# Kernel optimization log

Measured on AMD Instinct MI355X. Metric: run time of the kernel, lower is better.

The kernel has to match this reference:

```python
import jax, jax.numpy as jnp
import numpy as np

B, I, H = 16384, 512, 512


def setup_inputs() -> dict:
    key = jax.random.key(0)
    ks = jax.random.split(key, 10)
    inputs = jax.random.normal(ks[0], (B, I), dtype=jnp.float32)
    state = jax.random.normal(ks[1], (B, 2 * H), dtype=jnp.float32)
    # xavier_uniform for w_ih: U(-a, a), a = sqrt(6 / (fan_in + fan_out))
    a = float(np.sqrt(6.0 / (2 * H + I)))
    w_ih = jax.random.uniform(ks[2], (2 * H, I), jnp.float32, -a, a)
    b_h = jnp.zeros((H,), jnp.float32)
    pi = float(np.pi)
    d1 = jax.random.uniform(ks[3], (H,), jnp.float32, -pi, pi)
    d2 = jax.random.uniform(ks[4], (H,), jnp.float32, -pi, pi)
    d3 = jax.random.uniform(ks[5], (H,), jnp.float32, -pi, pi)
    re1 = jax.random.uniform(ks[6], (H,), jnp.float32, -1.0, 1.0)
    im1 = jax.random.uniform(ks[7], (H,), jnp.float32, -1.0, 1.0)
    re2 = jax.random.uniform(ks[8], (H,), jnp.float32, -1.0, 1.0)
    im2 = jax.random.uniform(ks[9], (H,), jnp.float32, -1.0, 1.0)
    perm = jnp.asarray(np.random.default_rng(0).permutation(H), dtype=jnp.int32)
    return {"inputs": inputs, "state": state, "w_ih": w_ih, "b_h": b_h,
            "d1": d1, "d2": d2, "d3": d3,
            "re1": re1, "im1": im1, "re2": re2, "im2": im2, "perm": perm}


def _diag_mul(w, z):
    # multiply by exp(i*w) built as complex(cos w, sin w), as in the original
    return jax.lax.complex(jnp.cos(w), jnp.sin(w)) * z


def _reflect(re, im, z):
    # z - (2/||v||^2) * (z @ conj(v)) outer v   (faithful to original matmuls)
    v = jax.lax.complex(re, im)                 # [H]
    vz = z @ jnp.conj(v)                        # [B]
    factor = 2.0 / jnp.sum(re * re + im * im)   # real scalar
    return z - factor * vz[:, None] * v[None, :]


def _modrelu(z, b):
    norm = jnp.abs(z)
    scale = jax.nn.relu(norm + b) / (norm + 1e-6)
    return z * scale


def reference(inputs, state, w_ih, b_h, d1, d2, d3, re1, im1, re2, im2, perm):
    inputs_mul = inputs @ w_ih.T                                  # [B, 2H]
    z_in = jax.lax.complex(inputs_mul[:, :H], inputs_mul[:, H:])  # [B, H] c64
    state_c = jax.lax.complex(state[:, :H], state[:, H:])
    # Unitary chain (computed in original forward, but its result `preact` is
    # never used for the returned state -- faithfully reproduced).
    s = _diag_mul(d1, state_c)
    s = jnp.fft.fft(s, axis=-1)
    s = _reflect(re1, im1, s)
    s = s[:, perm]                 # column permutation (z.T[P].T)
    s = _diag_mul(d2, s)
    s = jnp.fft.ifft(s, axis=-1)
    s = _reflect(re2, im2, s)
    s = _diag_mul(d3, s)
    preact = z_in + s              # dead in original; kept for fidelity
    new_state_c = _modrelu(z_in, b_h)
    return jnp.concatenate([jnp.real(new_state_c), jnp.imag(new_state_c)], axis=1)
```

## Files before the change

### kernel.cpp

```cpp
#include <hip/hip_runtime.h>
#include <hip/hip_bf16.h>


typedef __attribute__((ext_vector_type(8))) short bf16x8;
typedef __attribute__((ext_vector_type(4))) float f32x4;

#define BM 128
#define BK 64
#define KDIM 512
#define NDIM 1024
#define NKT 8

#define VMCNT(n) asm volatile("s_waitcnt vmcnt(" #n ")" ::: "memory")
#define LGKM(n)  asm volatile("s_waitcnt lgkmcnt(" #n ")" ::: "memory")

__device__ __forceinline__ unsigned short f2bf(float f) {
    unsigned u = __builtin_bit_cast(unsigned, f);
    u += 0x7fffu + ((u >> 16) & 1u);
    return (unsigned short)(u >> 16);
}

__global__ __launch_bounds__(256) void cvt_w(const float* __restrict__ W,
                                             unsigned short* __restrict__ Wbf, int n4) {
    int i = blockIdx.x * blockDim.x + threadIdx.x;
    int stride = gridDim.x * blockDim.x;
    for (; i < n4; i += stride) {
        float4 v = reinterpret_cast<const float4*>(W)[i];
        ushort4 o;
        o.x = f2bf(v.x); o.y = f2bf(v.y); o.z = f2bf(v.z); o.w = f2bf(v.w);
        reinterpret_cast<ushort4*>(Wbf)[i] = o;
    }
}

__device__ __forceinline__ void gload_lds16(const void* g, void* l) {
    __builtin_amdgcn_global_load_lds(
        (const __attribute__((address_space(1))) unsigned int*)g,
        (__attribute__((address_space(3))) unsigned int*)l, 16, 0, 0);
}

__device__ __forceinline__ unsigned cvtpk(float lo, float hi) {
    unsigned r;
    asm("v_cvt_pk_bf16_f32 %0, %1, %2" : "=v"(r) : "v"(lo), "v"(hi));
    return r;
}

__global__ __launch_bounds__(256, 2) void gemm_modrelu(
    const float* __restrict__ A,
    const unsigned short* __restrict__ W,
    const float* __restrict__ bh,
    float* __restrict__ out)
{
    __shared__ unsigned short At[2][BM * BK];
    __shared__ unsigned short Bt[2][BM * BK];

    const int tid = threadIdx.x;
    const int w   = tid >> 6;
    const int l   = tid & 63;
    const int l15 = l & 15;
    const int l4  = l >> 4;
    const int wm  = w >> 1;
    const int wn  = w & 1;

    const int bx = blockIdx.x;
    const int lg = (bx & 7) * 128 + (bx >> 3);
    const int mb = lg >> 3;
    const int cb = lg & 7;

    const int arow0 = tid >> 4;
    const int aseg  = tid & 15;
    const int aswz  = (arow0 & 7) << 3;
    const float4* gA = reinterpret_cast<const float4*>(A) + (size_t)(mb * BM) * (KDIM / 4);
    const int abase = arow0 * (KDIM / 4) + aseg;

    const int srow = l >> 3;
    const int sseg = (l & 7) ^ srow;
    const unsigned short* gb[4];
    int ldso[4];
#pragma unroll
    for (int is = 0; is < 4; ++is) {
        int row  = w * 32 + is * 8 + srow;
        int wrow = (row >> 6) * 512 + cb * 64 + (row & 63);
        gb[is]   = W + (size_t)wrow * KDIM + sseg * 8;
        ldso[is] = (w * 32 + is * 8) * BK;
    }

    float4 ra[3][8];
    auto load_a = [&](int kt, int set) {
#pragma unroll
        for (int s = 0; s < 8; ++s)
            ra[set][s] = gA[(size_t)s * 16 * (KDIM / 4) + abase + kt * (BK / 4)];
    };
    auto write_a = [&](int buf, int set) {
#pragma unroll
        for (int s = 0; s < 8; ++s) {
            uint2 o;
            o.x = cvtpk(ra[set][s].x, ra[set][s].y);
            o.y = cvtpk(ra[set][s].z, ra[set][s].w);
            int row = s * 16 + arow0;
            *reinterpret_cast<uint2*>(&At[buf][row * BK + ((aseg * 4) ^ aswz)]) = o;
        }
    };
    auto stage_b = [&](int kt, int buf) {
#pragma unroll
        for (int is = 0; is < 4; ++is)
            gload_lds16(gb[is] + kt * BK, &Bt[buf][ldso[is]]);
    };

    f32x4 acc[4][4];
#pragma unroll
    for (int i = 0; i < 4; ++i)
#pragma unroll
        for (int j = 0; j < 4; ++j) acc[i][j] = f32x4{0.f, 0.f, 0.f, 0.f};

    load_a(0, 0);
    load_a(1, 1);
    stage_b(0, 0);
    load_a(2, 2);
    stage_b(1, 1);
    VMCNT(24);
    write_a(0, 0);
    VMCNT(12);
    LGKM(0);
    __builtin_amdgcn_s_barrier();

#pragma unroll
    for (int kt = 0; kt < NKT; ++kt) {
        const int buf = kt & 1;

        bf16x8 af[4], bf[4];
#pragma unroll
        for (int i = 0; i < 4; ++i) {
            int row = wm * 64 + i * 16 + l15;
            af[i] = *(const bf16x8*)(&At[buf][row * BK + (l4 ^ (row & 7)) * 8]);
        }
#pragma unroll
        for (int j = 0; j < 4; ++j) {
            int row = (j >> 1) * 64 + wn * 32 + (j & 1) * 16 + l15;
            bf[j] = *(const bf16x8*)(&Bt[buf][row * BK + (l4 ^ (row & 7)) * 8]);
        }
        if (kt + 1 < NKT) write_a(buf ^ 1, (kt + 1) % 3);
        if (kt + 3 < NKT) load_a(kt + 3, (kt + 3) % 3);

        if (kt + 1 < NKT) { LGKM(8); } else { LGKM(0); }
        __builtin_amdgcn_sched_barrier(0);
        __builtin_amdgcn_s_setprio(1);
#pragma unroll
        for (int i = 0; i < 4; ++i)
#pragma unroll
            for (int j = 0; j < 4; ++j)
                acc[i][j] = __builtin_amdgcn_mfma_f32_16x16x32_bf16(
                    af[i], bf[j], acc[i][j], 0, 0, 0);
        __builtin_amdgcn_s_setprio(0);

#pragma unroll
        for (int i = 0; i < 4; ++i) {
            int row = wm * 64 + i * 16 + l15;
            af[i] = *(const bf16x8*)(&At[buf][row * BK + ((4 + l4) ^ (row & 7)) * 8]);
        }
#pragma unroll
        for (int j = 0; j < 4; ++j) {
            int row = (j >> 1) * 64 + wn * 32 + (j & 1) * 16 + l15;
            bf[j] = *(const bf16x8*)(&Bt[buf][row * BK + ((4 + l4) ^ (row & 7)) * 8]);
        }
        LGKM(0);
        __builtin_amdgcn_sched_barrier(0);
        __builtin_amdgcn_s_setprio(1);
#pragma unroll
        for (int i = 0; i < 4; ++i)
#pragma unroll
            for (int j = 0; j < 4; ++j)
                acc[i][j] = __builtin_amdgcn_mfma_f32_16x16x32_bf16(
                    af[i], bf[j], acc[i][j], 0, 0, 0);
        __builtin_amdgcn_s_setprio(0);

        if (kt + 1 < NKT) {
            __builtin_amdgcn_s_barrier();
            if (kt <= 4) { VMCNT(8); } else { VMCNT(0); }
            if (kt + 2 < NKT) stage_b(kt + 2, buf);
            __builtin_amdgcn_s_barrier();
        }
    }

#pragma unroll
    for (int jn = 0; jn < 2; ++jn) {
        int n = cb * 64 + wn * 32 + jn * 16 + l15;
        float b = bh[n];
#pragma unroll
        for (int i = 0; i < 4; ++i) {
#pragma unroll
            for (int j = 0; j < 4; ++j) {
                int m = mb * BM + wm * 64 + i * 16 + l4 * 4 + j;
                float re  = acc[i][jn][j];
                float imv = acc[i][jn + 2][j];
                float norm  = sqrtf(re * re + imv * imv);
                float scale = fmaxf(norm + b, 0.f) * __builtin_amdgcn_rcpf(norm + 1e-6f);
                float* po = out + (size_t)m * NDIM + n;
                __builtin_nontemporal_store(re  * scale, po);
                __builtin_nontemporal_store(imv * scale, po + 512);
            }
        }
    }
}

extern "C" void kernel_launch(void* const* d_in, const int* in_sizes, int n_in,
                              void* d_out, int out_size, void* d_ws, size_t ws_size,
                              hipStream_t stream) {
    const float* inputs = (const float*)d_in[0];
    const float* w_ih   = (const float*)d_in[2];
    const float* b_h    = (const float*)d_in[3];
    float* out = (float*)d_out;

    unsigned short* Wbf = (unsigned short*)d_ws;

    cvt_w<<<256, 256, 0, stream>>>(w_ih, Wbf, (1024 * 512) / 4);

    gemm_modrelu<<<1024, 256, 0, stream>>>(inputs, Wbf, b_h, out);
}
```

Measured before the change: 41.57 us.

## Triple-buffer B tiles with one barrier per k-step and stage output through LDS

B tiles move from two LDS buffers to three, so the async B load for step kt+2 is issued alongside the A-tile writes, and each k-iteration needs a single barrier instead of two. The epilogue no longer writes scalar nontemporal stores straight from the MFMA accumulators. It writes the modReLU results to an 80KB LDS scratch and then emits coalesced 16-byte vector stores. The larger LDS footprint and the dropped min-2-blocks launch bound may lower occupancy, and the extra LDS round trip adds epilogue latency.

Result: slower. 62.39 us (+50.1%).

```diff
diff --git a/kernel.cpp b/kernel.cpp
--- a/kernel.cpp
+++ b/kernel.cpp
@@ -44,14 +44,16 @@
     return r;
 }
 
-__global__ __launch_bounds__(256, 2) void gemm_modrelu(
+__global__ __launch_bounds__(256) void gemm_modrelu(
     const float* __restrict__ A,
     const unsigned short* __restrict__ W,
     const float* __restrict__ bh,
     float* __restrict__ out)
 {
-    __shared__ unsigned short At[2][BM * BK];
-    __shared__ unsigned short Bt[2][BM * BK];
+    __shared__ __align__(16) char smem[81920];
+    unsigned short* At0 = (unsigned short*)smem;
+    unsigned short* Bt0 = (unsigned short*)(smem + 32768);
+    float* C = (float*)smem;
 
     const int tid = threadIdx.x;
     const int w   = tid >> 6;
@@ -68,27 +70,26 @@
 
     const int arow0 = tid >> 4;
     const int aseg  = tid & 15;
-    const int aswz  = (arow0 & 7) << 3;
+    const int awoff = (aseg * 4) ^ ((arow0 & 7) << 3);
     const float4* gA = reinterpret_cast<const float4*>(A) + (size_t)(mb * BM) * (KDIM / 4);
-    const int abase = arow0 * (KDIM / 4) + aseg;
 
     const int srow = l >> 3;
     const int sseg = (l & 7) ^ srow;
     const unsigned short* gb[4];
-    int ldso[4];
+    int ldsoB[4];
 #pragma unroll
     for (int is = 0; is < 4; ++is) {
-        int row  = w * 32 + is * 8 + srow;
-        int wrow = (row >> 6) * 512 + cb * 64 + (row & 63);
-        gb[is]   = W + (size_t)wrow * KDIM + sseg * 8;
-        ldso[is] = (w * 32 + is * 8) * BK;
+        int row   = w * 32 + is * 8 + srow;
+        int wrow  = (row >> 6) * 512 + cb * 64 + (row & 63);
+        gb[is]    = W + (size_t)wrow * KDIM + sseg * 8;
+        ldsoB[is] = (w * 32 + is * 8) * BK;
     }
 
     float4 ra[3][8];
     auto load_a = [&](int kt, int set) {
 #pragma unroll
         for (int s = 0; s < 8; ++s)
-            ra[set][s] = gA[(size_t)s * 16 * (KDIM / 4) + abase + kt * (BK / 4)];
+            ra[set][s] = gA[(size_t)(s * 16 + arow0) * (KDIM / 4) + kt * (BK / 4) + aseg];
     };
     auto write_a = [&](int buf, int set) {
 #pragma unroll
@@ -96,14 +97,13 @@
             uint2 o;
             o.x = cvtpk(ra[set][s].x, ra[set][s].y);
             o.y = cvtpk(ra[set][s].z, ra[set][s].w);
-            int row = s * 16 + arow0;
-            *reinterpret_cast<uint2*>(&At[buf][row * BK + ((aseg * 4) ^ aswz)]) = o;
+            *reinterpret_cast<uint2*>(&At0[buf * 8192 + (s * 16 + arow0) * BK + awoff]) = o;
         }
     };
-    auto stage_b = [&](int kt, int buf) {
+    auto stage_b = [&](int kt, int bi) {
 #pragma unroll
         for (int is = 0; is < 4; ++is)
-            gload_lds16(gb[is] + kt * BK, &Bt[buf][ldso[is]]);
+            gload_lds16(gb[is] + kt * BK, Bt0 + bi * 8192 + ldsoB[is]);
     };
 
     f32x4 acc[4][4];
@@ -113,55 +113,38 @@
         for (int j = 0; j < 4; ++j) acc[i][j] = f32x4{0.f, 0.f, 0.f, 0.f};
 
     load_a(0, 0);
+    stage_b(0, 0);
     load_a(1, 1);
-    stage_b(0, 0);
+    stage_b(1, 1);
     load_a(2, 2);
-    stage_b(1, 1);
-    VMCNT(24);
+    VMCNT(20);
     write_a(0, 0);
-    VMCNT(12);
     LGKM(0);
-    __builtin_amdgcn_s_barrier();
+    __syncthreads();
 
 #pragma unroll
     for (int kt = 0; kt < NKT; ++kt) {
-        const int buf = kt & 1;
-
-        bf16x8 af[4], bf[4];
+        const unsigned short* at = At0 + (kt & 1) * 8192;
+        const unsigned short* bt = Bt0 + (kt % 3) * 8192;
+
+        if (kt <= 5)      { VMCNT(12); }
+        else if (kt == 6) { VMCNT(4); }
+
+        bf16x8 af[4], bfr[4];
 #pragma unroll
         for (int i = 0; i < 4; ++i) {
             int row = wm * 64 + i * 16 + l15;
-            af[i] = *(const bf16x8*)(&At[buf][row * BK + (l4 ^ (row & 7)) * 8]);
+            af[i] = *(const bf16x8*)(&at[row * BK + ((l4 ^ (row & 7)) * 8)]);
         }
 #pragma unroll
         for (int j = 0; j < 4; ++j) {
             int row = (j >> 1) * 64 + wn * 32 + (j & 1) * 16 + l15;
-            bf[j] = *(const bf16x8*)(&Bt[buf][row * BK + (l4 ^ (row & 7)) * 8]);
-        }
-        if (kt + 1 < NKT) write_a(buf ^ 1, (kt + 1) % 3);
+            bfr[j] = *(const bf16x8*)(&bt[row * BK + ((l4 ^ (row & 7)) * 8)]);
+        }
+        if (kt + 1 < NKT) write_a((kt + 1) & 1, (kt + 1) % 3);
+        if (kt + 2 < NKT) stage_b(kt + 2, (kt + 2) % 3);
         if (kt + 3 < NKT) load_a(kt + 3, (kt + 3) % 3);
 
-        if (kt + 1 < NKT) { LGKM(8); } else { LGKM(0); }
-        __builtin_amdgcn_sched_barrier(0);
-        __builtin_amdgcn_s_setprio(1);
-#pragma unroll
-        for (int i = 0; i < 4; ++i)
-#pragma unroll
-            for (int j = 0; j < 4; ++j)
-                acc[i][j] = __builtin_amdgcn_mfma_f32_16x16x32_bf16(
-                    af[i], bf[j], acc[i][j], 0, 0, 0);
-        __builtin_amdgcn_s_setprio(0);
-
-#pragma unroll
-        for (int i = 0; i < 4; ++i) {
-            int row = wm * 64 + i * 16 + l15;
-            af[i] = *(const bf16x8*)(&At[buf][row * BK + ((4 + l4) ^ (row & 7)) * 8]);
-        }
-#pragma unroll
-        for (int j = 0; j < 4; ++j) {
-            int row = (j >> 1) * 64 + wn * 32 + (j & 1) * 16 + l15;
-            bf[j] = *(const bf16x8*)(&Bt[buf][row * BK + ((4 + l4) ^ (row & 7)) * 8]);
-        }
         LGKM(0);
         __builtin_amdgcn_sched_barrier(0);
         __builtin_amdgcn_s_setprio(1);
@@ -170,35 +153,66 @@
 #pragma unroll
             for (int j = 0; j < 4; ++j)
                 acc[i][j] = __builtin_amdgcn_mfma_f32_16x16x32_bf16(
-                    af[i], bf[j], acc[i][j], 0, 0, 0);
+                    af[i], bfr[j], acc[i][j], 0, 0, 0);
         __builtin_amdgcn_s_setprio(0);
 
-        if (kt + 1 < NKT) {
-            __builtin_amdgcn_s_barrier();
-            if (kt <= 4) { VMCNT(8); } else { VMCNT(0); }
-            if (kt + 2 < NKT) stage_b(kt + 2, buf);
-            __builtin_amdgcn_s_barrier();
-        }
-    }
-
-#pragma unroll
-    for (int jn = 0; jn < 2; ++jn) {
-        int n = cb * 64 + wn * 32 + jn * 16 + l15;
-        float b = bh[n];
 #pragma unroll
         for (int i = 0; i < 4; ++i) {
-#pragma unroll
-            for (int j = 0; j < 4; ++j) {
-                int m = mb * BM + wm * 64 + i * 16 + l4 * 4 + j;
-                float re  = acc[i][jn][j];
-                float imv = acc[i][jn + 2][j];
+            int row = wm * 64 + i * 16 + l15;
+            af[i] = *(const bf16x8*)(&at[row * BK + (((4 + l4) ^ (row & 7)) * 8)]);
+        }
+#pragma unroll
+        for (int j = 0; j < 4; ++j) {
+            int row = (j >> 1) * 64 + wn * 32 + (j & 1) * 16 + l15;
+            bfr[j] = *(const bf16x8*)(&bt[row * BK + (((4 + l4) ^ (row & 7)) * 8)]);
+        }
+        LGKM(0);
+        __builtin_amdgcn_sched_barrier(0);
+        __builtin_amdgcn_s_setprio(1);
+#pragma unroll
+        for (int i = 0; i < 4; ++i)
+#pragma unroll
+            for (int j = 0; j < 4; ++j)
+                acc[i][j] = __builtin_amdgcn_mfma_f32_16x16x32_bf16(
+                    af[i], bfr[j], acc[i][j], 0, 0, 0);
+        __builtin_amdgcn_s_setprio(0);
+
+        if (kt <= 4)      { VMCNT(20); __builtin_amdgcn_s_barrier(); }
+        else if (kt == 5) { VMCNT(12); __builtin_amdgcn_s_barrier(); }
+        else if (kt == 6) { VMCNT(0);  __builtin_amdgcn_s_barrier(); }
+    }
+
+    __syncthreads();
+#pragma unroll
+    for (int j = 0; j < 2; ++j) {
+        int col = wn * 32 + j * 16 + l15;
+        float b = bh[cb * 64 + col];
+#pragma unroll
+        for (int i = 0; i < 4; ++i) {
+#pragma unroll
+            for (int jj = 0; jj < 4; ++jj) {
+                int rowl = wm * 64 + i * 16 + l4 * 4 + jj;
+                float re  = acc[i][j][jj];
+                float imv = acc[i][j + 2][jj];
                 float norm  = sqrtf(re * re + imv * imv);
                 float scale = fmaxf(norm + b, 0.f) * __builtin_amdgcn_rcpf(norm + 1e-6f);
-                float* po = out + (size_t)m * NDIM + n;
-                __builtin_nontemporal_store(re  * scale, po);
-                __builtin_nontemporal_store(imv * scale, po + 512);
+                C[rowl * 128 + col]      = re  * scale;
+                C[rowl * 128 + 64 + col] = imv * scale;
             }
         }
+    }
+    __syncthreads();
+
+    const int seg   = l & 31;
+    const int rhalf = l >> 5;
+#pragma unroll
+    for (int it = 0; it < 16; ++it) {
+        int rowl = w * 32 + it * 2 + rhalf;
+        f32x4 v = *reinterpret_cast<const f32x4*>(&C[rowl * 128 + seg * 4]);
+        size_t m = (size_t)(mb * BM + rowl);
+        int n = (seg < 16) ? (cb * 64 + seg * 4)
+                           : (512 + cb * 64 + (seg - 16) * 4);
+        *reinterpret_cast<f32x4*>(out + m * NDIM + n) = v;
     }
 }
 
```
